# Performance work log

Hardware: AMD Instinct MI355X
Metric: run time of the kernel (lower is better)

## Reference

```python
import jax, jax.numpy as jnp
import numpy as np

INPUT_DIM = 512
OUTPUT_DIM = 512
NUM_BASIS = 16
GRID_MIN, GRID_MAX = -2.0, 2.0
LN_EPS = 1e-5


def rbf_basis(x):
    # x: [batch, input_dim] -> [batch, input_dim, num_basis]
    centers = jnp.linspace(GRID_MIN, GRID_MAX, NUM_BASIS, dtype=x.dtype)  # [K]
    h = (GRID_MAX - GRID_MIN) / (NUM_BASIS - 1)
    z = (x[..., None] - centers) / h
    return jnp.exp(-(z * z))


def setup_inputs() -> dict:
    key = jax.random.key(0)
    k1, k2, k3 = jax.random.split(key, 3)
    x = jax.random.normal(k1, (4096, INPUT_DIM), dtype=jnp.float32)
    weights = jax.random.normal(k2, (OUTPUT_DIM, INPUT_DIM, NUM_BASIS), dtype=jnp.float32) * 0.1
    base_weights = jax.random.normal(k3, (OUTPUT_DIM, INPUT_DIM), dtype=jnp.float32) * 0.1
    ln_gamma = jnp.ones((OUTPUT_DIM,), dtype=jnp.float32)
    ln_beta = jnp.zeros((OUTPUT_DIM,), dtype=jnp.float32)
    return {"x": x, "weights": weights, "base_weights": base_weights,
            "ln_gamma": ln_gamma, "ln_beta": ln_beta}


def reference(x, weights, base_weights, ln_gamma, ln_beta):
    # per-edge basis expansion: [B, I, K]
    basis = rbf_basis(x)
    # fused contraction replacing the nested python loops:
    # out[b, j] = sum_{i,k} basis[b, i, k] * weights[j, i, k]
    out = jnp.einsum('bik,jik->bj', basis, weights)
    # residual base activation path
    out = out + jax.nn.silu(x) @ base_weights.T
    # layer norm over output_dim
    mean = jnp.mean(out, axis=-1, keepdims=True)
    var = jnp.var(out, axis=-1, keepdims=True)
    out = (out - mean) * jax.lax.rsqrt(var + LN_EPS) * ln_gamma + ln_beta
    return out
```

## Files before the change

### kernel.cpp

```cpp
#include <hip/hip_runtime.h>
#include <hip/hip_bf16.h>


typedef __bf16 bf16x8 __attribute__((ext_vector_type(8)));
typedef __bf16 bf16x4 __attribute__((ext_vector_type(4)));
typedef float  f32x4  __attribute__((ext_vector_type(4)));

#define KT 8704
#define SPLITS 8
#define KS (KT / SPLITS)
#define CPE (4096 * 512)

__device__ __forceinline__ void gll16(const __bf16* g, __bf16* l) {
    __builtin_amdgcn_global_load_lds(
        (const __attribute__((address_space(1))) void*)g,
        (__attribute__((address_space(3))) void*)l, 16, 0, 0);
}

__global__ void prep_AB(const float* __restrict__ x, const float* __restrict__ W,
                        const float* __restrict__ Wb, __bf16* __restrict__ A,
                        __bf16* __restrict__ B) {
    if (blockIdx.x < 8192) {
        int t = blockIdx.x * 256 + threadIdx.x;
        int b = t >> 9;
        int i = t & 511;
        float xv = x[t];
        float zb = 3.75f * xv + 7.5f;
        bf16x8 lo, hi;
#pragma unroll
        for (int k = 0; k < 8; ++k) { float z = zb - (float)k; lo[k]   = (__bf16)__expf(-z * z); }
#pragma unroll
        for (int k = 8; k < 16; ++k){ float z = zb - (float)k; hi[k-8] = (__bf16)__expf(-z * z); }
        size_t base = (size_t)b * KT + (size_t)i * 16;
        *(bf16x8*)(A + base)     = lo;
        *(bf16x8*)(A + base + 8) = hi;
        float s = xv / (1.0f + __expf(-xv));
        A[(size_t)b * KT + 8192 + i] = (__bf16)s;
    } else {
        int t = (blockIdx.x - 8192) * 256 + threadIdx.x;
        int j = t / 2176;
        int c = (t - j * 2176) * 4;
        float4 v;
        if (c < 8192) v = *(const float4*)&W[(size_t)j * 8192 + c];
        else          v = *(const float4*)&Wb[(size_t)j * 512 + (c - 8192)];
        bf16x4 o;
        o[0] = (__bf16)v.x; o[1] = (__bf16)v.y; o[2] = (__bf16)v.z; o[3] = (__bf16)v.w;
        *(bf16x4*)&B[(size_t)j * KT + c] = o;
    }
}

__global__ __launch_bounds__(256, 4) void gemm_bt(const __bf16* __restrict__ A,
                                                  const __bf16* __restrict__ B,
                                                  __bf16* __restrict__ Cp) {
    __shared__ __attribute__((aligned(16))) __bf16 As[128 * 32];
    __shared__ __attribute__((aligned(16))) __bf16 Bs[128 * 32];

    const int tid  = threadIdx.x;
    const int wave = tid >> 6, lane = tid & 63;
    const int q    = lane >> 4, r16 = lane & 15;
    const int m0 = blockIdx.x * 128, n0 = blockIdx.y * 128, k0 = blockIdx.z * KS;
    const int wm = wave & 1, wn = wave >> 1;

    const int row0 = tid >> 2, qk0 = (tid & 3) ^ ((row0 >> 1) & 3);
    const int row1 = row0 + 64, qk1 = (tid & 3) ^ ((row1 >> 1) & 3);
    const __bf16* gA0 = A + (size_t)(m0 + row0) * KT + k0 + qk0 * 8;
    const __bf16* gA1 = A + (size_t)(m0 + row1) * KT + k0 + qk1 * 8;
    const __bf16* gB0 = B + (size_t)(n0 + row0) * KT + k0 + qk0 * 8;
    const __bf16* gB1 = B + (size_t)(n0 + row1) * KT + k0 + qk1 * 8;
    __bf16* lA0 = &As[tid * 8];
    __bf16* lA1 = &As[(tid + 256) * 8];
    __bf16* lB0 = &Bs[tid * 8];
    __bf16* lB1 = &Bs[(tid + 256) * 8];

    f32x4 acc[4][4] = {};

    const int qa = q ^ ((r16 >> 1) & 3);
    const __bf16* Aw = &As[(wm * 64 + r16) * 32 + qa * 8];
    const __bf16* Bw = &Bs[(wn * 64 + r16) * 32 + qa * 8];

    for (int it = 0; it < KS / 32; ++it) {
        const int ko = it * 32;
        gll16(gA0 + ko, lA0);
        gll16(gA1 + ko, lA1);
        gll16(gB0 + ko, lB0);
        gll16(gB1 + ko, lB1);
        __syncthreads();

        bf16x8 af[4], bg[4];
#pragma unroll
        for (int mi = 0; mi < 4; ++mi) af[mi] = *(const bf16x8*)(Aw + mi * 512);
#pragma unroll
        for (int ni = 0; ni < 4; ++ni) bg[ni] = *(const bf16x8*)(Bw + ni * 512);
#pragma unroll
        for (int mi = 0; mi < 4; ++mi)
#pragma unroll
            for (int ni = 0; ni < 4; ++ni)
                acc[mi][ni] = __builtin_amdgcn_mfma_f32_16x16x32_bf16(
                    af[mi], bg[ni], acc[mi][ni], 0, 0, 0);
        __syncthreads();
    }

    __bf16* Cb = Cp + (size_t)blockIdx.z * CPE;
#pragma unroll
    for (int mi = 0; mi < 4; ++mi) {
        const int row = m0 + wm * 64 + mi * 16 + q * 4;
#pragma unroll
        for (int ni = 0; ni < 4; ++ni) {
            const int col = n0 + wn * 64 + ni * 16 + r16;
#pragma unroll
            for (int r = 0; r < 4; ++r)
                Cb[(size_t)(row + r) * 512 + col] = (__bf16)acc[mi][ni][r];
        }
    }
}

__global__ void ln_kernel(const __bf16* __restrict__ Cp, const float* __restrict__ gamma,
                          const float* __restrict__ beta, float* __restrict__ out) {
    const int tid  = threadIdx.x;
    const int wave = tid >> 6, lane = tid & 63;
    const int row  = blockIdx.x * 4 + wave;
    const size_t base = (size_t)row * 512 + lane * 8;

    float v[8] = {};
    float s = 0.f, s2 = 0.f;
#pragma unroll
    for (int z = 0; z < SPLITS; ++z) {
        bf16x8 p = *(const bf16x8*)(Cp + (size_t)z * CPE + base);
#pragma unroll
        for (int j = 0; j < 8; ++j) v[j] += (float)p[j];
    }
#pragma unroll
    for (int j = 0; j < 8; ++j) { s += v[j]; s2 += v[j] * v[j]; }
#pragma unroll
    for (int m = 32; m >= 1; m >>= 1) {
        s  += __shfl_xor(s, m);
        s2 += __shfl_xor(s2, m);
    }
    const float mean = s * (1.0f / 512.0f);
    const float var  = s2 * (1.0f / 512.0f) - mean * mean;
    const float rs   = rsqrtf(var + 1e-5f);
    float4 o0, o1;
    const float4 g0 = *(const float4*)&gamma[lane * 8];
    const float4 g1 = *(const float4*)&gamma[lane * 8 + 4];
    const float4 b0 = *(const float4*)&beta[lane * 8];
    const float4 b1 = *(const float4*)&beta[lane * 8 + 4];
    o0.x = (v[0] - mean) * rs * g0.x + b0.x;
    o0.y = (v[1] - mean) * rs * g0.y + b0.y;
    o0.z = (v[2] - mean) * rs * g0.z + b0.z;
    o0.w = (v[3] - mean) * rs * g0.w + b0.w;
    o1.x = (v[4] - mean) * rs * g1.x + b1.x;
    o1.y = (v[5] - mean) * rs * g1.y + b1.y;
    o1.z = (v[6] - mean) * rs * g1.z + b1.z;
    o1.w = (v[7] - mean) * rs * g1.w + b1.w;
    *(float4*)&out[base]     = o0;
    *(float4*)&out[base + 4] = o1;
}

extern "C" void kernel_launch(void* const* d_in, const int* in_sizes, int n_in,
                              void* d_out, int out_size, void* d_ws, size_t ws_size,
                              hipStream_t stream) {
    const float* x     = (const float*)d_in[0];
    const float* W     = (const float*)d_in[1];
    const float* Wb    = (const float*)d_in[2];
    const float* gamma = (const float*)d_in[3];
    const float* beta  = (const float*)d_in[4];
    float* out = (float*)d_out;

    char* ws = (char*)d_ws;
    __bf16* A  = (__bf16*)ws;
    __bf16* Bm = (__bf16*)(ws + 71303168);
    __bf16* Cp = (__bf16*)(ws + 80216064);

    prep_AB<<<8192 + 4352, 256, 0, stream>>>(x, W, Wb, A, Bm);
    dim3 g(32, 4, SPLITS);
    gemm_bt<<<g, 256, 0, stream>>>(A, Bm, Cp);
    ln_kernel<<<1024, 256, 0, stream>>>(Cp, gamma, beta, out);
}
```

Measured before the change: 148.9 us.

## Use K-slab layout, load B fragments directly from global, double-buffer A in LDS

Operand matrices are repacked into K-slabs of 32 columns so each GEMM step reads contiguous 64-byte rows. B fragments are now loaded straight from global/L2 into registers rather than staged through LDS, and A is double-buffered in LDS so the next slab's async load overlaps the current MFMAs. Prep indexing changes to match, and silu moves to a separate branch using a fast reciprocal. This cuts LDS traffic and halves the barriers per step, but B reads now depend on cache hits and their latency is no longer hidden by the LDS staging.

```diff
diff --git a/kernel.cpp b/kernel.cpp
--- a/kernel.cpp
+++ b/kernel.cpp
@@ -6,10 +6,12 @@
 typedef __bf16 bf16x4 __attribute__((ext_vector_type(4)));
 typedef float  f32x4  __attribute__((ext_vector_type(4)));
 
-#define KT 8704
 #define SPLITS 8
-#define KS (KT / SPLITS)
+#define NIT 34
 #define CPE (4096 * 512)
+#define LBUF (128 * 32)
+#define ASLAB 131072
+#define BSLAB 16384
 
 __device__ __forceinline__ void gll16(const __bf16* g, __bf16* l) {
     __builtin_amdgcn_global_load_lds(
@@ -17,27 +19,46 @@
         (__attribute__((address_space(3))) void*)l, 16, 0, 0);
 }
 
-__global__ void prep_AB(const float* __restrict__ x, const float* __restrict__ W,
-                        const float* __restrict__ Wb, __bf16* __restrict__ A,
-                        __bf16* __restrict__ B) {
-    if (blockIdx.x < 8192) {
-        int t = blockIdx.x * 256 + threadIdx.x;
-        int b = t >> 9;
-        int i = t & 511;
-        float xv = x[t];
-        float zb = 3.75f * xv + 7.5f;
-        bf16x8 lo, hi;
-#pragma unroll
-        for (int k = 0; k < 8; ++k) { float z = zb - (float)k; lo[k]   = (__bf16)__expf(-z * z); }
-#pragma unroll
-        for (int k = 8; k < 16; ++k){ float z = zb - (float)k; hi[k-8] = (__bf16)__expf(-z * z); }
-        size_t base = (size_t)b * KT + (size_t)i * 16;
-        *(bf16x8*)(A + base)     = lo;
-        *(bf16x8*)(A + base + 8) = hi;
-        float s = xv / (1.0f + __expf(-xv));
-        A[(size_t)b * KT + 8192 + i] = (__bf16)s;
+__device__ __forceinline__ float fsilu(float t) {
+    return t * __builtin_amdgcn_rcpf(1.0f + __expf(-t));
+}
+
+__global__ void prep_all(const float* __restrict__ x, const float* __restrict__ W,
+                         const float* __restrict__ Wb, __bf16* __restrict__ A2,
+                         __bf16* __restrict__ B2) {
+    const int blk = blockIdx.x, tid = threadIdx.x;
+    if (blk < 4096) {
+        int t = blk * 256 + tid;
+        int b = t & 4095, ip = t >> 12;
+        float x0 = x[(size_t)b * 512 + 2 * ip];
+        float x1 = x[(size_t)b * 512 + 2 * ip + 1];
+        float zb0 = 3.75f * x0 + 7.5f, zb1 = 3.75f * x1 + 7.5f;
+        bf16x8 v0, v1, v2, v3;
+#pragma unroll
+        for (int j = 0; j < 8; ++j) {
+            float d0 = zb0 - (float)j;       v0[j] = (__bf16)__expf(-d0 * d0);
+            float d1 = zb0 - (float)(j + 8); v1[j] = (__bf16)__expf(-d1 * d1);
+            float d2 = zb1 - (float)j;       v2[j] = (__bf16)__expf(-d2 * d2);
+            float d3 = zb1 - (float)(j + 8); v3[j] = (__bf16)__expf(-d3 * d3);
+        }
+        __bf16* p = A2 + ((size_t)ip * 4096 + b) * 32;
+        *(bf16x8*)(p)      = v0;
+        *(bf16x8*)(p + 8)  = v1;
+        *(bf16x8*)(p + 16) = v2;
+        *(bf16x8*)(p + 24) = v3;
+    } else if (blk < 4096 + 1024) {
+        int t = (blk - 4096) * 256 + tid;
+        int b = t >> 6, c = (t & 63) * 8;
+        float4 a0 = *(const float4*)&x[(size_t)b * 512 + c];
+        float4 a1 = *(const float4*)&x[(size_t)b * 512 + c + 4];
+        bf16x8 v;
+        v[0] = (__bf16)fsilu(a0.x); v[1] = (__bf16)fsilu(a0.y);
+        v[2] = (__bf16)fsilu(a0.z); v[3] = (__bf16)fsilu(a0.w);
+        v[4] = (__bf16)fsilu(a1.x); v[5] = (__bf16)fsilu(a1.y);
+        v[6] = (__bf16)fsilu(a1.z); v[7] = (__bf16)fsilu(a1.w);
+        *(bf16x8*)(A2 + ((size_t)(256 + (c >> 5)) * 4096 + b) * 32 + (c & 31)) = v;
     } else {
-        int t = (blockIdx.x - 8192) * 256 + threadIdx.x;
+        int t = (blk - 5120) * 256 + tid;
         int j = t / 2176;
         int c = (t - j * 2176) * 4;
         float4 v;
@@ -45,62 +66,69 @@
         else          v = *(const float4*)&Wb[(size_t)j * 512 + (c - 8192)];
         bf16x4 o;
         o[0] = (__bf16)v.x; o[1] = (__bf16)v.y; o[2] = (__bf16)v.z; o[3] = (__bf16)v.w;
-        *(bf16x4*)&B[(size_t)j * KT + c] = o;
-    }
-}
-
-__global__ __launch_bounds__(256, 4) void gemm_bt(const __bf16* __restrict__ A,
-                                                  const __bf16* __restrict__ B,
-                                                  __bf16* __restrict__ Cp) {
-    __shared__ __attribute__((aligned(16))) __bf16 As[128 * 32];
-    __shared__ __attribute__((aligned(16))) __bf16 Bs[128 * 32];
+        *(bf16x4*)(B2 + ((size_t)(c >> 5) * 512 + j) * 32 + (c & 31)) = o;
+    }
+}
+
+__global__ __launch_bounds__(256) void gemm_hyb(const __bf16* __restrict__ A2,
+                                                const __bf16* __restrict__ B2,
+                                                __bf16* __restrict__ Cp) {
+    __shared__ __attribute__((aligned(16))) __bf16 As[2 * LBUF];
 
     const int tid  = threadIdx.x;
     const int wave = tid >> 6, lane = tid & 63;
     const int q    = lane >> 4, r16 = lane & 15;
-    const int m0 = blockIdx.x * 128, n0 = blockIdx.y * 128, k0 = blockIdx.z * KS;
+    const int m0 = blockIdx.x * 128, n0 = blockIdx.y * 128;
+    const int bz = blockIdx.z, slab0 = bz * NIT;
     const int wm = wave & 1, wn = wave >> 1;
 
     const int row0 = tid >> 2, qk0 = (tid & 3) ^ ((row0 >> 1) & 3);
     const int row1 = row0 + 64, qk1 = (tid & 3) ^ ((row1 >> 1) & 3);
-    const __bf16* gA0 = A + (size_t)(m0 + row0) * KT + k0 + qk0 * 8;
-    const __bf16* gA1 = A + (size_t)(m0 + row1) * KT + k0 + qk1 * 8;
-    const __bf16* gB0 = B + (size_t)(n0 + row0) * KT + k0 + qk0 * 8;
-    const __bf16* gB1 = B + (size_t)(n0 + row1) * KT + k0 + qk1 * 8;
+    const __bf16* gA0 = A2 + (size_t)slab0 * ASLAB + (size_t)(m0 + row0) * 32 + qk0 * 8;
+    const __bf16* gA1 = A2 + (size_t)slab0 * ASLAB + (size_t)(m0 + row1) * 32 + qk1 * 8;
     __bf16* lA0 = &As[tid * 8];
     __bf16* lA1 = &As[(tid + 256) * 8];
-    __bf16* lB0 = &Bs[tid * 8];
-    __bf16* lB1 = &Bs[(tid + 256) * 8];
+
+    const __bf16* bBase = B2 + (size_t)slab0 * BSLAB
+                        + (size_t)(n0 + wn * 64 + r16) * 32 + q * 8;
 
     f32x4 acc[4][4] = {};
-
     const int qa = q ^ ((r16 >> 1) & 3);
-    const __bf16* Aw = &As[(wm * 64 + r16) * 32 + qa * 8];
-    const __bf16* Bw = &Bs[(wn * 64 + r16) * 32 + qa * 8];
-
-    for (int it = 0; it < KS / 32; ++it) {
-        const int ko = it * 32;
-        gll16(gA0 + ko, lA0);
-        gll16(gA1 + ko, lA1);
-        gll16(gB0 + ko, lB0);
-        gll16(gB1 + ko, lB1);
-        __syncthreads();
-
-        bf16x8 af[4], bg[4];
+    const int awOff = r16 * 32 + qa * 8 + wm * 64 * 32;
+
+    gll16(gA0, lA0);
+    gll16(gA1, lA1);
+    __syncthreads();
+
+    for (int it = 0; it < NIT; ++it) {
+        bf16x8 bg[4];
+        const __bf16* bp = bBase + (size_t)it * BSLAB;
+#pragma unroll
+        for (int ni = 0; ni < 4; ++ni) bg[ni] = *(const bf16x8*)(bp + ni * 512);
+
+        if (it + 1 < NIT) {
+            const size_t go = (size_t)(it + 1) * ASLAB;
+            const int sb = ((it + 1) & 1) * LBUF;
+            gll16(gA0 + go, &As[sb] + (lA0 - As));
+            gll16(gA1 + go, &As[sb] + (lA1 - As));
+        }
+
+        const __bf16* Aw = &As[(it & 1) * LBUF + awOff];
+        bf16x8 af[4];
 #pragma unroll
         for (int mi = 0; mi < 4; ++mi) af[mi] = *(const bf16x8*)(Aw + mi * 512);
-#pragma unroll
-        for (int ni = 0; ni < 4; ++ni) bg[ni] = *(const bf16x8*)(Bw + ni * 512);
+
 #pragma unroll
         for (int mi = 0; mi < 4; ++mi)
 #pragma unroll
             for (int ni = 0; ni < 4; ++ni)
                 acc[mi][ni] = __builtin_amdgcn_mfma_f32_16x16x32_bf16(
                     af[mi], bg[ni], acc[mi][ni], 0, 0, 0);
+
         __syncthreads();
     }
 
-    __bf16* Cb = Cp + (size_t)blockIdx.z * CPE;
+    __bf16* Cb = Cp + (size_t)bz * CPE;
 #pragma unroll
     for (int mi = 0; mi < 4; ++mi) {
         const int row = m0 + wm * 64 + mi * 16 + q * 4;
@@ -125,9 +153,9 @@
     float s = 0.f, s2 = 0.f;
 #pragma unroll
     for (int z = 0; z < SPLITS; ++z) {
-        bf16x8 p = *(const bf16x8*)(Cp + (size_t)z * CPE + base);
-#pragma unroll
-        for (int j = 0; j < 8; ++j) v[j] += (float)p[j];
+        bf16x8 pv = *(const bf16x8*)(Cp + (size_t)z * CPE + base);
+#pragma unroll
+        for (int j = 0; j < 8; ++j) v[j] += (float)pv[j];
     }
 #pragma unroll
     for (int j = 0; j < 8; ++j) { s += v[j]; s2 += v[j] * v[j]; }
@@ -167,12 +195,12 @@
     float* out = (float*)d_out;
 
     char* ws = (char*)d_ws;
-    __bf16* A  = (__bf16*)ws;
-    __bf16* Bm = (__bf16*)(ws + 71303168);
+    __bf16* A2 = (__bf16*)ws;
+    __bf16* B2 = (__bf16*)(ws + 71303168);
     __bf16* Cp = (__bf16*)(ws + 80216064);
 
-    prep_AB<<<8192 + 4352, 256, 0, stream>>>(x, W, Wb, A, Bm);
+    prep_all<<<4096 + 1024 + 4352, 256, 0, stream>>>(x, W, Wb, A2, B2);
     dim3 g(32, 4, SPLITS);
-    gemm_bt<<<g, 256, 0, stream>>>(A, Bm, Cp);
+    gemm_hyb<<<g, 256, 0, stream>>>(A2, B2, Cp);
     ln_kernel<<<1024, 256, 0, stream>>>(Cp, gamma, beta, out);
 }
```

Result: slower. 165.1 us (+10.9%).

## Load GEMM fragments directly from global memory, dropping LDS staging and barriers

Applied to the files above, without the earlier changes.

The split-K GEMM no longer stages A and B tiles through LDS with global_load_lds and two barriers per K step. Each wave now loads its MFMA fragments straight from global memory into registers, and the loop is unrolled by two. This removes the barrier stalls and LDS traffic, but each tile is now fetched separately by both waves that share it, which doubles L2 traffic. The per-lane 16-byte loads across rows strided by KT are also poorly coalesced. SiLU in the prep kernel now uses a fast reciprocal instead of a division.

```diff
diff --git a/kernel.cpp b/kernel.cpp
--- a/kernel.cpp
+++ b/kernel.cpp
@@ -8,13 +8,11 @@
 
 #define KT 8704
 #define SPLITS 8
-#define KS (KT / SPLITS)
+#define NIT 34
 #define CPE (4096 * 512)
 
-__device__ __forceinline__ void gll16(const __bf16* g, __bf16* l) {
-    __builtin_amdgcn_global_load_lds(
-        (const __attribute__((address_space(1))) void*)g,
-        (__attribute__((address_space(3))) void*)l, 16, 0, 0);
+__device__ __forceinline__ float fsilu(float t) {
+    return t * __builtin_amdgcn_rcpf(1.0f + __expf(-t));
 }
 
 __global__ void prep_AB(const float* __restrict__ x, const float* __restrict__ W,
@@ -34,8 +32,7 @@
         size_t base = (size_t)b * KT + (size_t)i * 16;
         *(bf16x8*)(A + base)     = lo;
         *(bf16x8*)(A + base + 8) = hi;
-        float s = xv / (1.0f + __expf(-xv));
-        A[(size_t)b * KT + 8192 + i] = (__bf16)s;
+        A[(size_t)b * KT + 8192 + i] = (__bf16)fsilu(xv);
     } else {
         int t = (blockIdx.x - 8192) * 256 + threadIdx.x;
         int j = t / 2176;
@@ -49,58 +46,39 @@
     }
 }
 
-__global__ __launch_bounds__(256, 4) void gemm_bt(const __bf16* __restrict__ A,
-                                                  const __bf16* __restrict__ B,
-                                                  __bf16* __restrict__ Cp) {
-    __shared__ __attribute__((aligned(16))) __bf16 As[128 * 32];
-    __shared__ __attribute__((aligned(16))) __bf16 Bs[128 * 32];
-
+__global__ __launch_bounds__(256) void gemm_direct(const __bf16* __restrict__ A,
+                                                   const __bf16* __restrict__ B,
+                                                   __bf16* __restrict__ Cp) {
     const int tid  = threadIdx.x;
     const int wave = tid >> 6, lane = tid & 63;
     const int q    = lane >> 4, r16 = lane & 15;
-    const int m0 = blockIdx.x * 128, n0 = blockIdx.y * 128, k0 = blockIdx.z * KS;
+    const int m0 = blockIdx.x * 128, n0 = blockIdx.y * 128;
+    const int bz = blockIdx.z, k0 = bz * 1088;
     const int wm = wave & 1, wn = wave >> 1;
 
-    const int row0 = tid >> 2, qk0 = (tid & 3) ^ ((row0 >> 1) & 3);
-    const int row1 = row0 + 64, qk1 = (tid & 3) ^ ((row1 >> 1) & 3);
-    const __bf16* gA0 = A + (size_t)(m0 + row0) * KT + k0 + qk0 * 8;
-    const __bf16* gA1 = A + (size_t)(m0 + row1) * KT + k0 + qk1 * 8;
-    const __bf16* gB0 = B + (size_t)(n0 + row0) * KT + k0 + qk0 * 8;
-    const __bf16* gB1 = B + (size_t)(n0 + row1) * KT + k0 + qk1 * 8;
-    __bf16* lA0 = &As[tid * 8];
-    __bf16* lA1 = &As[(tid + 256) * 8];
-    __bf16* lB0 = &Bs[tid * 8];
-    __bf16* lB1 = &Bs[(tid + 256) * 8];
+    const __bf16* aBase = A + (size_t)(m0 + wm * 64 + r16) * KT + k0 + q * 8;
+    const __bf16* bBase = B + (size_t)(n0 + wn * 64 + r16) * KT + k0 + q * 8;
 
     f32x4 acc[4][4] = {};
 
-    const int qa = q ^ ((r16 >> 1) & 3);
-    const __bf16* Aw = &As[(wm * 64 + r16) * 32 + qa * 8];
-    const __bf16* Bw = &Bs[(wn * 64 + r16) * 32 + qa * 8];
-
-    for (int it = 0; it < KS / 32; ++it) {
-        const int ko = it * 32;
-        gll16(gA0 + ko, lA0);
-        gll16(gA1 + ko, lA1);
-        gll16(gB0 + ko, lB0);
-        gll16(gB1 + ko, lB1);
-        __syncthreads();
-
+#pragma unroll 2
+    for (int it = 0; it < NIT; ++it) {
+        const __bf16* ap = aBase + it * 32;
+        const __bf16* bp = bBase + it * 32;
         bf16x8 af[4], bg[4];
 #pragma unroll
-        for (int mi = 0; mi < 4; ++mi) af[mi] = *(const bf16x8*)(Aw + mi * 512);
+        for (int mi = 0; mi < 4; ++mi) af[mi] = *(const bf16x8*)(ap + (size_t)(mi * 16) * KT);
 #pragma unroll
-        for (int ni = 0; ni < 4; ++ni) bg[ni] = *(const bf16x8*)(Bw + ni * 512);
+        for (int ni = 0; ni < 4; ++ni) bg[ni] = *(const bf16x8*)(bp + (size_t)(ni * 16) * KT);
 #pragma unroll
         for (int mi = 0; mi < 4; ++mi)
 #pragma unroll
             for (int ni = 0; ni < 4; ++ni)
                 acc[mi][ni] = __builtin_amdgcn_mfma_f32_16x16x32_bf16(
                     af[mi], bg[ni], acc[mi][ni], 0, 0, 0);
-        __syncthreads();
     }
 
-    __bf16* Cb = Cp + (size_t)blockIdx.z * CPE;
+    __bf16* Cb = Cp + (size_t)bz * CPE;
 #pragma unroll
     for (int mi = 0; mi < 4; ++mi) {
         const int row = m0 + wm * 64 + mi * 16 + q * 4;
@@ -125,9 +103,9 @@
     float s = 0.f, s2 = 0.f;
 #pragma unroll
     for (int z = 0; z < SPLITS; ++z) {
-        bf16x8 p = *(const bf16x8*)(Cp + (size_t)z * CPE + base);
+        bf16x8 pv = *(const bf16x8*)(Cp + (size_t)z * CPE + base);
 #pragma unroll
-        for (int j = 0; j < 8; ++j) v[j] += (float)p[j];
+        for (int j = 0; j < 8; ++j) v[j] += (float)pv[j];
     }
 #pragma unroll
     for (int j = 0; j < 8; ++j) { s += v[j]; s2 += v[j] * v[j]; }
@@ -173,6 +151,6 @@
 
     prep_AB<<<8192 + 4352, 256, 0, stream>>>(x, W, Wb, A, Bm);
     dim3 g(32, 4, SPLITS);
-    gemm_bt<<<g, 256, 0, stream>>>(A, Bm, Cp);
+    gemm_direct<<<g, 256, 0, stream>>>(A, Bm, Cp);
     ln_kernel<<<1024, 256, 0, stream>>>(Cp, gamma, beta, out);
 }
```

Result: slower. 227.5 us (+52.8%).
